# Optimization experiments

Hardware: AMD Instinct MI355X
Metric: run time of the kernel (lower is better)

Reference implementation:

```python
import jax, jax.numpy as jnp
import numpy as np

B, T, I, H, HOUT = 512, 256, 32, 128, 1
H2 = H // 2


def setup_inputs() -> dict:
    key = jax.random.key(0)
    ks = jax.random.split(key, 16)
    s = lambda *shape: 1.0 / np.sqrt(H)
    def u(k, shape):
        return jax.random.uniform(k, shape, jnp.float32, -1.0 / np.sqrt(H), 1.0 / np.sqrt(H))
    return {
        "x": jax.random.normal(ks[0], (B, T, I), jnp.float32),
        # layer 0 LSTM weights (PyTorch layout: [4H, in], gate order i,f,g,o)
        "w_ih0": u(ks[1], (4 * H, I)),
        "w_hh0": u(ks[2], (4 * H, H)),
        "b_ih0": u(ks[3], (4 * H,)),
        "b_hh0": u(ks[4], (4 * H,)),
        # layer 1 LSTM weights
        "w_ih1": u(ks[5], (4 * H, H)),
        "w_hh1": u(ks[6], (4 * H, H)),
        "b_ih1": u(ks[7], (4 * H,)),
        "b_hh1": u(ks[8], (4 * H,)),
        # MLP head: Linear(H, H//2) -> ReLU -> Linear(H//2, HOUT)
        "fc1_w": u(ks[9], (H2, H)),
        "fc1_b": u(ks[10], (H2,)),
        "fc2_w": u(ks[11], (HOUT, H2)),
        "fc2_b": u(ks[12], (HOUT,)),
    }


def _lstm_layer(x, w_ih, w_hh, b_ih, b_hh):
    # x: (B, T, in) -> h sequence (B, T, H). Dropout is eval-mode identity.
    b, t, _ = x.shape
    h_dim = w_hh.shape[1]
    # precompute input-to-gate projections for the whole sequence (one big GEMM)
    xg = jnp.einsum("bti,gi->btg", x, w_ih) + b_ih + b_hh  # (B, T, 4H)
    xg = jnp.swapaxes(xg, 0, 1)  # (T, B, 4H) for scan

    def step(carry, g_t):
        h, c = carry
        gates = g_t + h @ w_hh.T  # (B, 4H)
        i, f, g, o = jnp.split(gates, 4, axis=-1)  # PyTorch gate order i,f,g,o
        i = jax.nn.sigmoid(i)
        f = jax.nn.sigmoid(f)
        g = jnp.tanh(g)
        o = jax.nn.sigmoid(o)
        c_new = f * c + i * g
        h_new = o * jnp.tanh(c_new)
        return (h_new, c_new), h_new

    zeros = jnp.zeros((b, h_dim), x.dtype)
    _, hs = jax.lax.scan(step, (zeros, zeros), xg)
    return jnp.swapaxes(hs, 0, 1)  # (B, T, H)


def reference(x, w_ih0, w_hh0, b_ih0, b_hh0, w_ih1, w_hh1, b_ih1, b_hh1,
              fc1_w, fc1_b, fc2_w, fc2_b):
    h0 = _lstm_layer(x, w_ih0, w_hh0, b_ih0, b_hh0)   # (B, T, H)
    h1 = _lstm_layer(h0, w_ih1, w_hh1, b_ih1, b_hh1)  # (B, T, H)
    last = h1[:, -1, :]  # (B, H); dropout = identity in eval
    z = jax.nn.relu(last @ fc1_w.T + fc1_b)  # (B, H//2)
    return z @ fc2_w.T + fc2_b  # (B, forecast_horizon)
```

## Files before the change

### kernel.cpp

```cpp
#include <hip/hip_runtime.h>

#define NB 512
#define NT 256
#define NI 32
#define NH 128
#define NG 512

typedef __attribute__((ext_vector_type(8))) short bf16x8;
typedef __attribute__((ext_vector_type(4))) float f32x4;

__device__ __forceinline__ float fsig(float x) {
    return __builtin_amdgcn_rcpf(1.0f + __expf(-x));
}
__device__ __forceinline__ float ftanh(float x) {
    float e = __expf(-2.0f * x);
    return 2.0f * __builtin_amdgcn_rcpf(1.0f + e) - 1.0f;
}
__device__ __forceinline__ unsigned short f2bf_rne(float f) {
    unsigned u = __float_as_uint(f);
    return (unsigned short)((u + 0x7FFFu + ((u >> 16) & 1u)) >> 16);
}
__device__ __forceinline__ void split2(float a, float b, unsigned& hi, unsigned& lo) {
    unsigned short ha = f2bf_rne(a), hb = f2bf_rne(b);
    float ra = a - __uint_as_float((unsigned)ha << 16);
    float rb = b - __uint_as_float((unsigned)hb << 16);
    hi = (unsigned)ha | ((unsigned)hb << 16);
    lo = (unsigned)f2bf_rne(ra) | ((unsigned)f2bf_rne(rb) << 16);
}
__device__ __forceinline__ bf16x8 u4bf(uint4 u) {
    union { uint4 u; bf16x8 v; } c; c.u = u; return c.v;
}
#define MFMA16(accv, av, bv) \
    accv = __builtin_amdgcn_mfma_f32_16x16x32_bf16(av, bv, accv, 0, 0, 0)

__device__ __forceinline__ void lds_barrier() {
    asm volatile("s_waitcnt lgkmcnt(0)\n\ts_barrier" ::: "memory");
}

__global__ __launch_bounds__(512, 1)
void recur_pair(const float* __restrict__ xg0,
                const float* __restrict__ xg1,
                const float* __restrict__ w_hh0,
                const float* __restrict__ w_hh1,
                float* __restrict__ h0buf,
                float* __restrict__ h0s, float* __restrict__ c0s,
                float* __restrict__ h1s, float* __restrict__ c1s,
                int Tc, int doA, int doB, int firstA, int firstB)
{
    __shared__ __align__(16) unsigned short Hh[2][16][128];
    __shared__ __align__(16) unsigned short Hl[2][16][128];

    const int role = blockIdx.x >> 5;
    if (role == 0 && !doA) return;
    if (role == 1 && !doB) return;

    const float* xg    = role ? xg1   : xg0;
    const float* wsrc  = role ? w_hh1 : w_hh0;
    float*       hout  = role ? nullptr : h0buf;
    float*       hs    = role ? h1s : h0s;
    float*       cs    = role ? c1s : c0s;
    const int    first = role ? firstB : firstA;

    const int p    = blockIdx.x & 31;
    const int tid  = threadIdx.x;
    const int wv   = tid >> 6;
    const int lane = tid & 63;
    const int quad = lane >> 4;
    const int ml   = lane & 15;
    const int j    = 16 * wv + ml;

    bf16x8 wh[4][4], wl[4][4];
#pragma unroll
    for (int t = 0; t < 4; ++t) {
#pragma unroll
        for (int q = 0; q < 4; ++q) {
            int n = (t * 8 + wv) * 16 + ml;
            const float* s = wsrc + (size_t)n * NH + q * 32 + quad * 8;
            float4 v0 = *(const float4*)s;
            float4 v1 = *(const float4*)(s + 4);
            uint4 H, L;
            split2(v0.x, v0.y, H.x, L.x); split2(v0.z, v0.w, H.y, L.y);
            split2(v1.x, v1.y, H.z, L.z); split2(v1.z, v1.w, H.w, L.w);
            wh[t][q] = u4bf(H);
            wl[t][q] = u4bf(L);
        }
    }

    int ro[4];
#pragma unroll
    for (int q = 0; q < 4; ++q)
        ro[q] = ((ml * 256 + q * 64 + quad * 16) ^ ((ml & 7) << 4));
    int wo[4];
    size_t hb_r[4], sb_r[4];
#pragma unroll
    for (int r = 0; r < 4; ++r) {
        int m = quad * 4 + r;
        wo[r]   = ((m * 256 + j * 2) ^ ((m & 7) << 4));
        hb_r[r] = (size_t)(p * 16 + m) * Tc * NH + j;
        sb_r[r] = (size_t)(p * 16 + m) * NH + j;
    }

    const size_t rs = (size_t)Tc * NG;
    const size_t rowb0 = ((size_t)(p * 16 + quad * 4) * Tc) * NG + j;

    float xga[4][4], xgb[4][4];
#pragma unroll
    for (int t = 0; t < 4; ++t)
#pragma unroll
        for (int r = 0; r < 4; ++r)
            xga[t][r] = xg[rowb0 + (size_t)r * rs + t * 128];

    float cr[4];
#pragma unroll
    for (int r = 0; r < 4; ++r) {
        float h = 0.f, c = 0.f;
        if (!first) {
            h = hs[sb_r[r]];
            c = cs[sb_r[r]];
        }
        cr[r] = c;
        unsigned short hi = f2bf_rne(h);
        float res = h - __uint_as_float((unsigned)hi << 16);
        unsigned short lo = f2bf_rne(res);
        *(unsigned short*)((char*)&Hh[0][0][0] + wo[r]) = hi;
        *(unsigned short*)((char*)&Hl[0][0][0] + wo[r]) = lo;
    }
    __syncthreads();

    auto prefetch = [&](float (&dst)[4][4], int tlx) __attribute__((always_inline)) {
        int tc_ = tlx < Tc ? tlx : Tc - 1;
        const size_t rowb = rowb0 + (size_t)tc_ * NG;
#pragma unroll
        for (int t = 0; t < 4; ++t)
#pragma unroll
            for (int r = 0; r < 4; ++r)
                dst[t][r] = xg[rowb + (size_t)r * rs + t * 128];
    };

    auto step_body = [&](int TL, int BUF, const float (&xgv)[4][4]) __attribute__((always_inline)) {
        const char* hb = (const char*)&Hh[BUF][0][0];
        const char* lb = (const char*)&Hl[BUF][0][0];
        char* hbn = (char*)&Hh[BUF ^ 1][0][0];
        char* lbn = (char*)&Hl[BUF ^ 1][0][0];

        f32x4 acc[4] = {};
#pragma unroll
        for (int q = 0; q < 4; ++q) {
            bf16x8 ah = *(const bf16x8*)(hb + ro[q]);
            bf16x8 al = *(const bf16x8*)(lb + ro[q]);
#pragma unroll
            for (int t = 0; t < 4; ++t) {
                MFMA16(acc[t], ah, wh[t][q]);
                MFMA16(acc[t], al, wh[t][q]);
                MFMA16(acc[t], ah, wl[t][q]);
            }
        }

#pragma unroll
        for (int r = 0; r < 4; ++r) {
            float gi = fsig (acc[0][r] + xgv[0][r]);
            float gf = fsig (acc[1][r] + xgv[1][r]);
            float gg = ftanh(acc[2][r] + xgv[2][r]);
            float go = fsig (acc[3][r] + xgv[3][r]);
            cr[r] = gf * cr[r] + gi * gg;
            float hn = go * ftanh(cr[r]);
            unsigned short hi = f2bf_rne(hn);
            float res = hn - __uint_as_float((unsigned)hi << 16);
            unsigned short lo = f2bf_rne(res);
            *(unsigned short*)(hbn + wo[r]) = hi;
            *(unsigned short*)(lbn + wo[r]) = lo;
            if (hout)
                hout[hb_r[r] + (size_t)TL * NH] = hn;
            if (TL == Tc - 1) {
                hs[sb_r[r]] = hn;
                cs[sb_r[r]] = cr[r];
            }
        }
    };

    for (int tl = 0; tl < Tc; tl += 2) {
        prefetch(xgb, tl + 1);
        step_body(tl, 0, xga);
        lds_barrier();
        if (tl + 1 < Tc) {
            prefetch(xga, tl + 2);
            step_body(tl + 1, 1, xgb);
            lds_barrier();
        }
    }
}

template<int KP, bool SLICED>
__global__ __launch_bounds__(256)
void gemm_mfma(const float* __restrict__ A,
               const float* __restrict__ Bw,
               const float* __restrict__ bi, const float* __restrict__ bh,
               float* __restrict__ C, int t0, int tcShift)
{
    constexpr int K = KP * 32;
    __shared__ __align__(16) unsigned short Ah[4][128][8], Al[4][128][8];
    __shared__ __align__(16) unsigned short Bh[4][64][8],  Bl[4][64][8];
    const int tid  = threadIdx.x;
    const int n0   = blockIdx.x * 64;
    const int m0   = blockIdx.y * 128;
    const int wv   = tid >> 6;
    const int lane = tid & 63;
    const int quad = lane >> 4, ml = lane & 15;

    f32x4 acc[2][4] = {};
    float bias[4];
#pragma unroll
    for (int nt = 0; nt < 4; ++nt) {
        int n = n0 + nt * 16 + ml;
        bias[nt] = bi[n] + bh[n];
    }

    for (int kp = 0; kp < KP; ++kp) {
        if (kp) __syncthreads();
#pragma unroll
        for (int r = 0; r < 2; ++r) {
            int u = tid + 256 * r;
            int m = u >> 2, ck = u & 3;
            size_t abase;
            if (SLICED) {
                int mg = m0 + m;
                int b  = mg >> tcShift, tl = mg & ((1 << tcShift) - 1);
                abase = ((size_t)b * NT + (t0 + tl)) * K;
            } else {
                abase = (size_t)(m0 + m) * K;
            }
            const float* s = A + abase + kp * 32 + ck * 8;
            float4 v0 = *(const float4*)s;
            float4 v1 = *(const float4*)(s + 4);
            uint4 H, L;
            split2(v0.x, v0.y, H.x, L.x); split2(v0.z, v0.w, H.y, L.y);
            split2(v1.x, v1.y, H.z, L.z); split2(v1.z, v1.w, H.w, L.w);
            *(uint4*)&Ah[ck][m][0] = H;
            *(uint4*)&Al[ck][m][0] = L;
        }
        {
            int n = tid >> 2, ck = tid & 3;
            const float* s = Bw + (size_t)(n0 + n) * K + kp * 32 + ck * 8;
            float4 v0 = *(const float4*)s;
            float4 v1 = *(const float4*)(s + 4);
            uint4 H, L;
            split2(v0.x, v0.y, H.x, L.x); split2(v0.z, v0.w, H.y, L.y);
            split2(v1.x, v1.y, H.z, L.z); split2(v1.z, v1.w, H.w, L.w);
            *(uint4*)&Bh[ck][n][0] = H;
            *(uint4*)&Bl[ck][n][0] = L;
        }
        __syncthreads();

        bf16x8 ah0 = *(const bf16x8*)&Ah[quad][(2 * wv + 0) * 16 + ml][0];
        bf16x8 al0 = *(const bf16x8*)&Al[quad][(2 * wv + 0) * 16 + ml][0];
        bf16x8 ah1 = *(const bf16x8*)&Ah[quad][(2 * wv + 1) * 16 + ml][0];
        bf16x8 al1 = *(const bf16x8*)&Al[quad][(2 * wv + 1) * 16 + ml][0];
#pragma unroll
        for (int nt = 0; nt < 4; ++nt) {
            bf16x8 bhv = *(const bf16x8*)&Bh[quad][nt * 16 + ml][0];
            bf16x8 blv = *(const bf16x8*)&Bl[quad][nt * 16 + ml][0];
            MFMA16(acc[0][nt], ah0, bhv);
            MFMA16(acc[0][nt], ah0, blv);
            MFMA16(acc[0][nt], al0, bhv);
            MFMA16(acc[1][nt], ah1, bhv);
            MFMA16(acc[1][nt], ah1, blv);
            MFMA16(acc[1][nt], al1, bhv);
        }
    }

#pragma unroll
    for (int mt = 0; mt < 2; ++mt)
#pragma unroll
        for (int nt = 0; nt < 4; ++nt)
#pragma unroll
            for (int reg = 0; reg < 4; ++reg) {
                int m = m0 + (2 * wv + mt) * 16 + quad * 4 + reg;
                int n = n0 + nt * 16 + ml;
                C[(size_t)m * NG + n] = acc[mt][nt][reg] + bias[nt];
            }
}

__global__ void fc_head(const float* __restrict__ h1,
                        const float* __restrict__ fc1w, const float* __restrict__ fc1b,
                        const float* __restrict__ fc2w, const float* __restrict__ fc2b,
                        float* __restrict__ out)
{
    int b = blockIdx.x, j = threadIdx.x;
    const float4* wr = (const float4*)(fc1w + (size_t)j * NH);
    const float4* hv = (const float4*)(h1 + (size_t)b * NH);
    float acc = fc1b[j];
#pragma unroll
    for (int q = 0; q < 32; ++q) {
        float4 w = wr[q], h = hv[q];
        acc += w.x * h.x + w.y * h.y + w.z * h.z + w.w * h.w;
    }
    float z = fmaxf(acc, 0.0f);
    float p = fc2w[j] * z;
#pragma unroll
    for (int off = 32; off > 0; off >>= 1) p += __shfl_down(p, off);
    if (j == 0) out[b] = p + fc2b[0];
}

extern "C" void kernel_launch(void* const* d_in, const int* in_sizes, int n_in,
                              void* d_out, int out_size, void* d_ws, size_t ws_size,
                              hipStream_t stream)
{
    const float* x     = (const float*)d_in[0];
    const float* w_ih0 = (const float*)d_in[1];
    const float* w_hh0 = (const float*)d_in[2];
    const float* b_ih0 = (const float*)d_in[3];
    const float* b_hh0 = (const float*)d_in[4];
    const float* w_ih1 = (const float*)d_in[5];
    const float* w_hh1 = (const float*)d_in[6];
    const float* b_ih1 = (const float*)d_in[7];
    const float* b_hh1 = (const float*)d_in[8];
    const float* fc1w  = (const float*)d_in[9];
    const float* fc1b  = (const float*)d_in[10];
    const float* fc2w  = (const float*)d_in[11];
    const float* fc2b  = (const float*)d_in[12];
    float* out = (float*)d_out;
    float* ws  = (float*)d_ws;

    int Tc = 1;
    for (int cand = 256; cand >= 1; cand >>= 1) {
        size_t need = 4ull * ((size_t)NB * cand * (2 * NG + NH) + 4ull * NB * NH);
        if (need <= ws_size) { Tc = cand; break; }
    }
    int tcShift = __builtin_ctz((unsigned)Tc);

    size_t o_xg0 = 0;
    size_t o_xg1 = o_xg0 + (size_t)NB * Tc * NG;
    size_t o_h0  = o_xg1 + (size_t)NB * Tc * NG;
    size_t o_h0s = o_h0  + (size_t)NB * Tc * NH;
    size_t o_c0s = o_h0s + (size_t)NB * NH;
    size_t o_h1s = o_c0s + (size_t)NB * NH;
    size_t o_c1s = o_h1s + (size_t)NB * NH;

    const int M = NB * Tc;
    const int nchunk = NT / Tc;

    gemm_mfma<1, true><<<dim3(8, M / 128), 256, 0, stream>>>(
        x, w_ih0, b_ih0, b_hh0, ws + o_xg0, 0, tcShift);

    for (int i = 0; i <= nchunk; ++i) {
        int doA = (i < nchunk), doB = (i >= 1);
        recur_pair<<<64, 512, 0, stream>>>(
            ws + o_xg0, ws + o_xg1, w_hh0, w_hh1, ws + o_h0,
            ws + o_h0s, ws + o_c0s, ws + o_h1s, ws + o_c1s,
            Tc, doA, doB, i == 0, i == 1);
        if (i < nchunk)
            gemm_mfma<4, false><<<dim3(8, M / 128), 256, 0, stream>>>(
                ws + o_h0, w_ih1, b_ih1, b_hh1, ws + o_xg1, 0, 0);
        if (i + 1 < nchunk)
            gemm_mfma<1, true><<<dim3(8, M / 128), 256, 0, stream>>>(
                x, w_ih0, b_ih0, b_hh0, ws + o_xg0, (i + 1) * Tc, tcShift);
    }
    fc_head<<<NB, 64, 0, stream>>>(ws + o_h1s, fc1w, fc1b, fc2w, fc2b, out);
}
```

Baseline: 825.6 us.

## Fuse layer-0 input projection into recurrence and use exp2-scaled activations

Computes the layer-0 input projection inside the recurrent kernel using MFMA on x with W_ih0 staged in LDS, removing the separate xg0 GEMM and its workspace traffic. Weights and biases are prescaled by log2(e) so gates use exp2 with combined reciprocals, and MFMA accumulation is split across two accumulator sets to shorten dependency chains. The time chunk is capped at 32, which pipelines layer 0 and layer 1 across more launches but adds launch overhead and per-step MFMA work in layer 0.

```diff
diff --git a/kernel.cpp b/kernel.cpp
--- a/kernel.cpp
+++ b/kernel.cpp
@@ -6,16 +6,12 @@
 #define NH 128
 #define NG 512
 
+#define L2E  1.4426950408889634f
+#define L2E2 2.8853900817779268f
+
 typedef __attribute__((ext_vector_type(8))) short bf16x8;
 typedef __attribute__((ext_vector_type(4))) float f32x4;
 
-__device__ __forceinline__ float fsig(float x) {
-    return __builtin_amdgcn_rcpf(1.0f + __expf(-x));
-}
-__device__ __forceinline__ float ftanh(float x) {
-    float e = __expf(-2.0f * x);
-    return 2.0f * __builtin_amdgcn_rcpf(1.0f + e) - 1.0f;
-}
 __device__ __forceinline__ unsigned short f2bf_rne(float f) {
     unsigned u = __float_as_uint(f);
     return (unsigned short)((u + 0x7FFFu + ((u >> 16) & 1u)) >> 16);
@@ -37,26 +33,28 @@
     asm volatile("s_waitcnt lgkmcnt(0)\n\ts_barrier" ::: "memory");
 }
 
-__global__ __launch_bounds__(512, 1)
-void recur_pair(const float* __restrict__ xg0,
+__global__ __launch_bounds__(512, 2)
+void recur_pair(const float* __restrict__ x,
                 const float* __restrict__ xg1,
                 const float* __restrict__ w_hh0,
                 const float* __restrict__ w_hh1,
+                const float* __restrict__ w_ih0,
+                const float* __restrict__ b_ih0, const float* __restrict__ b_hh0,
                 float* __restrict__ h0buf,
                 float* __restrict__ h0s, float* __restrict__ c0s,
                 float* __restrict__ h1s, float* __restrict__ c1s,
-                int Tc, int doA, int doB, int firstA, int firstB)
+                int Tc, int doA, int doB, int firstA, int firstB, int t0A)
 {
     __shared__ __align__(16) unsigned short Hh[2][16][128];
     __shared__ __align__(16) unsigned short Hl[2][16][128];
+    __shared__ __align__(16) uint4 WIh[32][64];
+    __shared__ __align__(16) uint4 WIl[32][64];
 
     const int role = blockIdx.x >> 5;
     if (role == 0 && !doA) return;
     if (role == 1 && !doB) return;
 
-    const float* xg    = role ? xg1   : xg0;
     const float* wsrc  = role ? w_hh1 : w_hh0;
-    float*       hout  = role ? nullptr : h0buf;
     float*       hs    = role ? h1s : h0s;
     float*       cs    = role ? c1s : c0s;
     const int    first = role ? firstB : firstA;
@@ -72,6 +70,7 @@
     bf16x8 wh[4][4], wl[4][4];
 #pragma unroll
     for (int t = 0; t < 4; ++t) {
+        const float sc = (t == 2) ? L2E2 : L2E;
 #pragma unroll
         for (int q = 0; q < 4; ++q) {
             int n = (t * 8 + wv) * 16 + ml;
@@ -79,8 +78,8 @@
             float4 v0 = *(const float4*)s;
             float4 v1 = *(const float4*)(s + 4);
             uint4 H, L;
-            split2(v0.x, v0.y, H.x, L.x); split2(v0.z, v0.w, H.y, L.y);
-            split2(v1.x, v1.y, H.z, L.z); split2(v1.z, v1.w, H.w, L.w);
+            split2(v0.x * sc, v0.y * sc, H.x, L.x); split2(v0.z * sc, v0.w * sc, H.y, L.y);
+            split2(v1.x * sc, v1.y * sc, H.z, L.z); split2(v1.z * sc, v1.w * sc, H.w, L.w);
             wh[t][q] = u4bf(H);
             wl[t][q] = u4bf(L);
         }
@@ -99,16 +98,6 @@
         hb_r[r] = (size_t)(p * 16 + m) * Tc * NH + j;
         sb_r[r] = (size_t)(p * 16 + m) * NH + j;
     }
-
-    const size_t rs = (size_t)Tc * NG;
-    const size_t rowb0 = ((size_t)(p * 16 + quad * 4) * Tc) * NG + j;
-
-    float xga[4][4], xgb[4][4];
-#pragma unroll
-    for (int t = 0; t < 4; ++t)
-#pragma unroll
-        for (int r = 0; r < 4; ++r)
-            xga[t][r] = xg[rowb0 + (size_t)r * rs + t * 128];
 
     float cr[4];
 #pragma unroll
@@ -125,79 +114,188 @@
         *(unsigned short*)((char*)&Hh[0][0][0] + wo[r]) = hi;
         *(unsigned short*)((char*)&Hl[0][0][0] + wo[r]) = lo;
     }
-    __syncthreads();
-
-    auto prefetch = [&](float (&dst)[4][4], int tlx) __attribute__((always_inline)) {
-        int tc_ = tlx < Tc ? tlx : Tc - 1;
-        const size_t rowb = rowb0 + (size_t)tc_ * NG;
-#pragma unroll
-        for (int t = 0; t < 4; ++t)
-#pragma unroll
-            for (int r = 0; r < 4; ++r)
-                dst[t][r] = xg[rowb + (size_t)r * rs + t * 128];
+
+    auto activ = [&](float mi, float mf, float mg, float mo, float& c)
+        __attribute__((always_inline)) -> float {
+        float ei = exp2f(mi), ef = exp2f(mf), eg = exp2f(mg), eo = exp2f(mo);
+        float rf  = __builtin_amdgcn_rcpf(1.0f + ef);
+        float rig = __builtin_amdgcn_rcpf((1.0f + ei) * (1.0f + eg));
+        float cn  = c * rf + (1.0f - eg) * rig;
+        c = cn;
+        float ec = exp2f(cn * -L2E2);
+        float rh = __builtin_amdgcn_rcpf((1.0f + eo) * (1.0f + ec));
+        return (1.0f - ec) * rh;
     };
 
-    auto step_body = [&](int TL, int BUF, const float (&xgv)[4][4]) __attribute__((always_inline)) {
-        const char* hb = (const char*)&Hh[BUF][0][0];
-        const char* lb = (const char*)&Hl[BUF][0][0];
-        char* hbn = (char*)&Hh[BUF ^ 1][0][0];
-        char* lbn = (char*)&Hl[BUF ^ 1][0][0];
-
-        f32x4 acc[4] = {};
-#pragma unroll
-        for (int q = 0; q < 4; ++q) {
-            bf16x8 ah = *(const bf16x8*)(hb + ro[q]);
-            bf16x8 al = *(const bf16x8*)(lb + ro[q]);
+    if (role == 0) {
+#pragma unroll
+        for (int t = 0; t < 4; ++t) {
+            const float sc = (t == 2) ? L2E2 : L2E;
+            int n = (t * 8 + wv) * 16 + ml;
+            const float* s = w_ih0 + (size_t)n * NI + quad * 8;
+            float4 v0 = *(const float4*)s;
+            float4 v1 = *(const float4*)(s + 4);
+            uint4 H, L;
+            split2(v0.x * sc, v0.y * sc, H.x, L.x); split2(v0.z * sc, v0.w * sc, H.y, L.y);
+            split2(v1.x * sc, v1.y * sc, H.z, L.z); split2(v1.z * sc, v1.w * sc, H.w, L.w);
+            WIh[t * 8 + wv][lane] = H;
+            WIl[t * 8 + wv][lane] = L;
+        }
+        float nb[4];
+#pragma unroll
+        for (int t = 0; t < 4; ++t) {
+            const float sc = (t == 2) ? L2E2 : L2E;
+            int n = t * 128 + j;
+            nb[t] = -(b_ih0[n] + b_hh0[n]) * sc;
+        }
+        __syncthreads();
+
+        const float* xrow = x + (size_t)(p * 16 + ml) * NT * NI + quad * 8;
+        auto xload = [&](float4& a, float4& b, int TL) __attribute__((always_inline)) {
+            int tc_ = TL < Tc ? TL : Tc - 1;
+            const float* sp = xrow + (size_t)(t0A + tc_) * NI;
+            a = *(const float4*)sp;
+            b = *(const float4*)(sp + 4);
+        };
+
+        auto step0 = [&](int TL, int BUF, float4 x0, float4 x1)
+            __attribute__((always_inline)) {
+            const char* hb = (const char*)&Hh[BUF][0][0];
+            const char* lb = (const char*)&Hl[BUF][0][0];
+            char* hbn = (char*)&Hh[BUF ^ 1][0][0];
+            char* lbn = (char*)&Hl[BUF ^ 1][0][0];
+
+            uint4 XH, XL;
+            split2(x0.x, x0.y, XH.x, XL.x); split2(x0.z, x0.w, XH.y, XL.y);
+            split2(x1.x, x1.y, XH.z, XL.z); split2(x1.z, x1.w, XH.w, XL.w);
+            bf16x8 xh = u4bf(XH), xl = u4bf(XL);
+
+            f32x4 P[4] = {}, Q[4] = {};
 #pragma unroll
             for (int t = 0; t < 4; ++t) {
-                MFMA16(acc[t], ah, wh[t][q]);
-                MFMA16(acc[t], al, wh[t][q]);
-                MFMA16(acc[t], ah, wl[t][q]);
-            }
-        }
-
-#pragma unroll
-        for (int r = 0; r < 4; ++r) {
-            float gi = fsig (acc[0][r] + xgv[0][r]);
-            float gf = fsig (acc[1][r] + xgv[1][r]);
-            float gg = ftanh(acc[2][r] + xgv[2][r]);
-            float go = fsig (acc[3][r] + xgv[3][r]);
-            cr[r] = gf * cr[r] + gi * gg;
-            float hn = go * ftanh(cr[r]);
-            unsigned short hi = f2bf_rne(hn);
-            float res = hn - __uint_as_float((unsigned)hi << 16);
-            unsigned short lo = f2bf_rne(res);
-            *(unsigned short*)(hbn + wo[r]) = hi;
-            *(unsigned short*)(lbn + wo[r]) = lo;
-            if (hout)
-                hout[hb_r[r] + (size_t)TL * NH] = hn;
-            if (TL == Tc - 1) {
-                hs[sb_r[r]] = hn;
-                cs[sb_r[r]] = cr[r];
-            }
-        }
-    };
-
-    for (int tl = 0; tl < Tc; tl += 2) {
-        prefetch(xgb, tl + 1);
-        step_body(tl, 0, xga);
-        lds_barrier();
-        if (tl + 1 < Tc) {
+                bf16x8 wihh = u4bf(WIh[t * 8 + wv][lane]);
+                bf16x8 wihl = u4bf(WIl[t * 8 + wv][lane]);
+                MFMA16(P[t], xh, wihh);
+                MFMA16(Q[t], xl, wihh);
+                MFMA16(Q[t], xh, wihl);
+            }
+#pragma unroll
+            for (int q = 0; q < 4; ++q) {
+                bf16x8 ah = *(const bf16x8*)(hb + ro[q]);
+                bf16x8 al = *(const bf16x8*)(lb + ro[q]);
+#pragma unroll
+                for (int t = 0; t < 4; ++t) {
+                    MFMA16(P[t], ah, wh[t][q]);
+                    MFMA16(Q[t], al, wh[t][q]);
+                    if (q & 1) { MFMA16(P[t], ah, wl[t][q]); }
+                    else       { MFMA16(Q[t], ah, wl[t][q]); }
+                }
+            }
+#pragma unroll
+            for (int r = 0; r < 4; ++r) {
+                float mi = nb[0] - P[0][r] - Q[0][r];
+                float mf = nb[1] - P[1][r] - Q[1][r];
+                float mg = nb[2] - P[2][r] - Q[2][r];
+                float mo = nb[3] - P[3][r] - Q[3][r];
+                float hn = activ(mi, mf, mg, mo, cr[r]);
+                unsigned short hi = f2bf_rne(hn);
+                float res = hn - __uint_as_float((unsigned)hi << 16);
+                unsigned short lo = f2bf_rne(res);
+                *(unsigned short*)(hbn + wo[r]) = hi;
+                *(unsigned short*)(lbn + wo[r]) = lo;
+                h0buf[hb_r[r] + (size_t)TL * NH] = hn;
+                if (TL == Tc - 1) {
+                    hs[sb_r[r]] = hn;
+                    cs[sb_r[r]] = cr[r];
+                }
+            }
+        };
+
+        float4 xa0, xa1, xb0, xb1;
+        xload(xa0, xa1, 0);
+        for (int tl = 0; tl < Tc; tl += 2) {
+            xload(xb0, xb1, tl + 1);
+            step0(tl, 0, xa0, xa1);
+            lds_barrier();
+            xload(xa0, xa1, tl + 2);
+            step0(tl + 1, 1, xb0, xb1);
+            lds_barrier();
+        }
+    } else {
+        __syncthreads();
+
+        const size_t rs = (size_t)Tc * NG;
+        const size_t rowb0 = ((size_t)(p * 16 + quad * 4) * Tc) * NG + j;
+
+        auto prefetch = [&](float (&dst)[4][4], int tlx) __attribute__((always_inline)) {
+            int tc_ = tlx < Tc ? tlx : Tc - 1;
+            const size_t rowb = rowb0 + (size_t)tc_ * NG;
+#pragma unroll
+            for (int t = 0; t < 4; ++t)
+#pragma unroll
+                for (int r = 0; r < 4; ++r)
+                    dst[t][r] = xg1[rowb + (size_t)r * rs + t * 128];
+        };
+
+        auto step1 = [&](int TL, int BUF, const float (&xgv)[4][4])
+            __attribute__((always_inline)) {
+            const char* hb = (const char*)&Hh[BUF][0][0];
+            const char* lb = (const char*)&Hl[BUF][0][0];
+            char* hbn = (char*)&Hh[BUF ^ 1][0][0];
+            char* lbn = (char*)&Hl[BUF ^ 1][0][0];
+
+            f32x4 P[4] = {}, Q[4] = {};
+#pragma unroll
+            for (int q = 0; q < 4; ++q) {
+                bf16x8 ah = *(const bf16x8*)(hb + ro[q]);
+                bf16x8 al = *(const bf16x8*)(lb + ro[q]);
+#pragma unroll
+                for (int t = 0; t < 4; ++t) {
+                    MFMA16(P[t], ah, wh[t][q]);
+                    MFMA16(Q[t], al, wh[t][q]);
+                    if (q & 1) { MFMA16(P[t], ah, wl[t][q]); }
+                    else       { MFMA16(Q[t], ah, wl[t][q]); }
+                }
+            }
+#pragma unroll
+            for (int r = 0; r < 4; ++r) {
+                float mi = xgv[0][r] - P[0][r] - Q[0][r];
+                float mf = xgv[1][r] - P[1][r] - Q[1][r];
+                float mg = xgv[2][r] - P[2][r] - Q[2][r];
+                float mo = xgv[3][r] - P[3][r] - Q[3][r];
+                float hn = activ(mi, mf, mg, mo, cr[r]);
+                unsigned short hi = f2bf_rne(hn);
+                float res = hn - __uint_as_float((unsigned)hi << 16);
+                unsigned short lo = f2bf_rne(res);
+                *(unsigned short*)(hbn + wo[r]) = hi;
+                *(unsigned short*)(lbn + wo[r]) = lo;
+                if (TL == Tc - 1) {
+                    hs[sb_r[r]] = hn;
+                    cs[sb_r[r]] = cr[r];
+                }
+            }
+        };
+
+        float xga[4][4], xgb[4][4];
+        prefetch(xga, 0);
+        for (int tl = 0; tl < Tc; tl += 2) {
+            prefetch(xgb, tl + 1);
+            step1(tl, 0, xga);
+            lds_barrier();
             prefetch(xga, tl + 2);
-            step_body(tl + 1, 1, xgb);
+            step1(tl + 1, 1, xgb);
             lds_barrier();
         }
     }
 }
 
-template<int KP, bool SLICED>
 __global__ __launch_bounds__(256)
-void gemm_mfma(const float* __restrict__ A,
-               const float* __restrict__ Bw,
-               const float* __restrict__ bi, const float* __restrict__ bh,
-               float* __restrict__ C, int t0, int tcShift)
+void gemm_ih1(const float* __restrict__ A,
+              const float* __restrict__ Bw,
+              const float* __restrict__ bi, const float* __restrict__ bh,
+              float* __restrict__ C)
 {
-    constexpr int K = KP * 32;
+    constexpr int K = 128;
     __shared__ __align__(16) unsigned short Ah[4][128][8], Al[4][128][8];
     __shared__ __align__(16) unsigned short Bh[4][64][8],  Bl[4][64][8];
     const int tid  = threadIdx.x;
@@ -207,31 +305,24 @@
     const int lane = tid & 63;
     const int quad = lane >> 4, ml = lane & 15;
 
+    const float s = ((blockIdx.x >> 1) == 2) ? L2E2 : L2E;
     f32x4 acc[2][4] = {};
-    float bias[4];
+    float nbs[4];
 #pragma unroll
     for (int nt = 0; nt < 4; ++nt) {
         int n = n0 + nt * 16 + ml;
-        bias[nt] = bi[n] + bh[n];
-    }
-
-    for (int kp = 0; kp < KP; ++kp) {
+        nbs[nt] = -(bi[n] + bh[n]) * s;
+    }
+
+    for (int kp = 0; kp < 4; ++kp) {
         if (kp) __syncthreads();
 #pragma unroll
         for (int r = 0; r < 2; ++r) {
             int u = tid + 256 * r;
             int m = u >> 2, ck = u & 3;
-            size_t abase;
-            if (SLICED) {
-                int mg = m0 + m;
-                int b  = mg >> tcShift, tl = mg & ((1 << tcShift) - 1);
-                abase = ((size_t)b * NT + (t0 + tl)) * K;
-            } else {
-                abase = (size_t)(m0 + m) * K;
-            }
-            const float* s = A + abase + kp * 32 + ck * 8;
-            float4 v0 = *(const float4*)s;
-            float4 v1 = *(const float4*)(s + 4);
+            const float* sp = A + (size_t)(m0 + m) * K + kp * 32 + ck * 8;
+            float4 v0 = *(const float4*)sp;
+            float4 v1 = *(const float4*)(sp + 4);
             uint4 H, L;
             split2(v0.x, v0.y, H.x, L.x); split2(v0.z, v0.w, H.y, L.y);
             split2(v1.x, v1.y, H.z, L.z); split2(v1.z, v1.w, H.w, L.w);
@@ -240,9 +331,9 @@
         }
         {
             int n = tid >> 2, ck = tid & 3;
-            const float* s = Bw + (size_t)(n0 + n) * K + kp * 32 + ck * 8;
-            float4 v0 = *(const float4*)s;
-            float4 v1 = *(const float4*)(s + 4);
+            const float* sp = Bw + (size_t)(n0 + n) * K + kp * 32 + ck * 8;
+            float4 v0 = *(const float4*)sp;
+            float4 v1 = *(const float4*)(sp + 4);
             uint4 H, L;
             split2(v0.x, v0.y, H.x, L.x); split2(v0.z, v0.w, H.y, L.y);
             split2(v1.x, v1.y, H.z, L.z); split2(v1.z, v1.w, H.w, L.w);
@@ -276,7 +367,7 @@
             for (int reg = 0; reg < 4; ++reg) {
                 int m = m0 + (2 * wv + mt) * 16 + quad * 4 + reg;
                 int n = n0 + nt * 16 + ml;
-                C[(size_t)m * NG + n] = acc[mt][nt][reg] + bias[nt];
+                C[(size_t)m * NG + n] = fmaf(acc[mt][nt][reg], -s, nbs[nt]);
             }
 }
 
@@ -321,39 +412,29 @@
     float* out = (float*)d_out;
     float* ws  = (float*)d_ws;
 
-    int Tc = 1;
-    for (int cand = 256; cand >= 1; cand >>= 1) {
-        size_t need = 4ull * ((size_t)NB * cand * (2 * NG + NH) + 4ull * NB * NH);
-        if (need <= ws_size) { Tc = cand; break; }
-    }
-    int tcShift = __builtin_ctz((unsigned)Tc);
-
-    size_t o_xg0 = 0;
-    size_t o_xg1 = o_xg0 + (size_t)NB * Tc * NG;
+    int Tc = 32;
+    while (Tc > 1 &&
+           4ull * ((size_t)NB * Tc * (NG + NH) + 4ull * NB * NH) > ws_size)
+        Tc >>= 1;
+
+    size_t o_xg1 = 0;
     size_t o_h0  = o_xg1 + (size_t)NB * Tc * NG;
     size_t o_h0s = o_h0  + (size_t)NB * Tc * NH;
     size_t o_c0s = o_h0s + (size_t)NB * NH;
     size_t o_h1s = o_c0s + (size_t)NB * NH;
     size_t o_c1s = o_h1s + (size_t)NB * NH;
 
-    const int M = NB * Tc;
     const int nchunk = NT / Tc;
-
-    gemm_mfma<1, true><<<dim3(8, M / 128), 256, 0, stream>>>(
-        x, w_ih0, b_ih0, b_hh0, ws + o_xg0, 0, tcShift);
 
     for (int i = 0; i <= nchunk; ++i) {
         int doA = (i < nchunk), doB = (i >= 1);
         recur_pair<<<64, 512, 0, stream>>>(
-            ws + o_xg0, ws + o_xg1, w_hh0, w_hh1, ws + o_h0,
-            ws + o_h0s, ws + o_c0s, ws + o_h1s, ws + o_c1s,
-            Tc, doA, doB, i == 0, i == 1);
+            x, ws + o_xg1, w_hh0, w_hh1, w_ih0, b_ih0, b_hh0,
+            ws + o_h0, ws + o_h0s, ws + o_c0s, ws + o_h1s, ws + o_c1s,
+            Tc, doA, doB, i == 0, i == 1, i * Tc);
         if (i < nchunk)
-            gemm_mfma<4, false><<<dim3(8, M / 128), 256, 0, stream>>>(
-                ws + o_h0, w_ih1, b_ih1, b_hh1, ws + o_xg1, 0, 0);
-        if (i + 1 < nchunk)
-            gemm_mfma<1, true><<<dim3(8, M / 128), 256, 0, stream>>>(
-                x, w_ih0, b_ih0, b_hh0, ws + o_xg0, (i + 1) * Tc, tcShift);
+            gemm_ih1<<<dim3(8, NB * Tc / 128), 256, 0, stream>>>(
+                ws + o_h0, w_ih1, b_ih1, b_hh1, ws + o_xg1);
     }
     fc_head<<<NB, 64, 0, stream>>>(ws + o_h1s, fc1w, fc1b, fc2w, fc2b, out);
 }
```

Result: slower. 909.8 us (+10.2%).
